# Kernel tuning notes

Measured on AMD Instinct MI355X. Metric: run time of the kernel, lower is better.

The kernel has to match this reference:

```python
import jax, jax.numpy as jnp
import numpy as np


def setup_inputs() -> dict:
    key = jax.random.key(0)
    ks = jax.random.split(key, 12)
    N_DRUGS, D, N_CELLS, C_IN, E = 4096, 128, 1024, 1000, 500000
    inp = {
        "drug_hidden_out": jax.random.normal(ks[0], (N_DRUGS, D), dtype=jnp.float32),
        "cell_hidden_out": jax.random.normal(ks[1], (N_CELLS, C_IN), dtype=jnp.float32),
        # columns: drug1_idx, drug2_idx, cell_idx, label (original code indexes
        # drug_hidden_out with ALL THREE index columns, so bound by N_DRUGS)
        "all_edges": jax.random.randint(ks[2], (E, 4), 0, N_DRUGS, dtype=jnp.int64),
        # proj: Linear(1000, 128)
        "proj_W": jax.random.normal(ks[3], (D, C_IN), dtype=jnp.float32) * 0.03,
        "proj_b": jnp.zeros((D,), dtype=jnp.float32),
        # NN: Linear(128,32) -> ReLU -> Linear(32,32) -> ReLU -> Linear(32,32)
        #     -> ReLU -> Dropout(eval=identity) -> Linear(32,1) -> Sigmoid
        "W1": jax.random.normal(ks[4], (32, D), dtype=jnp.float32) * 0.08,
        "b1": jnp.zeros((32,), dtype=jnp.float32),
        "W2": jax.random.normal(ks[5], (32, 32), dtype=jnp.float32) * 0.17,
        "b2": jnp.zeros((32,), dtype=jnp.float32),
        "W3": jax.random.normal(ks[6], (32, 32), dtype=jnp.float32) * 0.17,
        "b3": jnp.zeros((32,), dtype=jnp.float32),
        "W4": jax.random.normal(ks[7], (1, 32), dtype=jnp.float32) * 0.17,
        "b4": jnp.zeros((1,), dtype=jnp.float32),
    }
    return inp


def reference(drug_hidden_out, cell_hidden_out, all_edges,
              proj_W, proj_b, W1, b1, W2, b2, W3, b3, W4, b4):
    # proj is computed in the original forward but its result is never used
    # downstream (the code re-indexes drug_hidden_out for cell_fea).
    _cell_proj = cell_hidden_out @ proj_W.T + proj_b  # [n_cells, 128], dead value

    edges = all_edges.T                 # [4, E]
    label = edges[3]                    # [E]
    edge_index = edges[:3]              # [3, E]

    drug1_fea = drug_hidden_out[edge_index[0]]   # [E, 128] gather
    drug2_fea = drug_hidden_out[edge_index[1]]   # [E, 128] gather
    cell_fea = drug_hidden_out[edge_index[2]]    # [E, 128] gather (faithful to source bug)
    logits = drug1_fea * drug2_fea * cell_fea    # [E, 128]

    h = jax.nn.relu(logits @ W1.T + b1)          # [E, 32]
    h = jax.nn.relu(h @ W2.T + b2)               # [E, 32]
    h = jax.nn.relu(h @ W3.T + b3)               # [E, 32] (dropout = identity in eval)
    x = jax.nn.sigmoid(h @ W4.T + b4)            # [E, 1]
    return x, label
```

## Files before the change

### kernel.cpp

```cpp
#include <hip/hip_runtime.h>
#include <stdint.h>

#define DD 128
#define HH 32
#define TABQ (4096 * DD / 4)
#define BLOB_OFF (1u << 20)

typedef _Float16 f16;
typedef _Float16 f16x2 __attribute__((ext_vector_type(2)));
typedef _Float16 f16x4 __attribute__((ext_vector_type(4)));
typedef _Float16 f16x8 __attribute__((ext_vector_type(8)));
typedef float    f32x4 __attribute__((ext_vector_type(4)));
typedef uint32_t u32x4 __attribute__((ext_vector_type(4)));

#define GL1(p)  ((const __attribute__((address_space(1))) void*)(p))
#define LDS3(p) ((__attribute__((address_space(3))) void*)(p))

__global__ __launch_bounds__(256)
void synergy_prepass(const float* __restrict__ drug,
                     const float* __restrict__ W1, const float* __restrict__ W2,
                     const float* __restrict__ W3, const float* __restrict__ W4,
                     f16* __restrict__ tab)
{
    const int tid = threadIdx.x;
    if ((int)blockIdx.x == 512) {
        f16x8* __restrict__ blob16 = (f16x8*)((char*)tab + BLOB_OFF);
        const float4* __restrict__ W1v = (const float4*)W1;
        #pragma unroll
        for (int p = 0; p < 2; ++p) {
            const int S = p * 256 + tid;
            const int t = S >> 8, f = (S >> 6) & 3, l = S & 63;
            const int mm = l & 15, qq = l >> 4;
            const int c4 = (t * 16 + mm) * (DD / 4) + f * 8 + qq * 2;
            const float4 w0 = W1v[c4], w1 = W1v[c4 + 1];
            f16x8 r;
            r[0]=(f16)w0.x; r[1]=(f16)w0.y; r[2]=(f16)w0.z; r[3]=(f16)w0.w;
            r[4]=(f16)w1.x; r[5]=(f16)w1.y; r[6]=(f16)w1.z; r[7]=(f16)w1.w;
            blob16[S] = r;
        }
        {
            const int B = tid & 127;
            const int t = B >> 6, l = B & 63;
            const int mm = l & 15, qq = l >> 4;
            const int c4 = (t * 16 + mm) * (HH / 4) + qq * 2;
            const float4* __restrict__ src = (tid < 128) ? (const float4*)W2 : (const float4*)W3;
            const float4 w0 = src[c4], w1 = src[c4 + 1];
            f16x8 r;
            r[0]=(f16)w0.x; r[1]=(f16)w0.y; r[2]=(f16)w0.z; r[3]=(f16)w0.w;
            r[4]=(f16)w1.x; r[5]=(f16)w1.y; r[6]=(f16)w1.z; r[7]=(f16)w1.w;
            blob16[512 + (tid & 128) + B] = r;
        }
        if (tid < 64) {
            const int mm = tid & 15, qq = tid >> 4;
            f16x8 r;
            #pragma unroll
            for (int j = 0; j < 8; ++j)
                r[j] = (mm == 0) ? (f16)W4[qq * 8 + j] : (f16)0.0f;
            blob16[768 + tid] = r;
        }
        return;
    }
    const int i = blockIdx.x * 256 + tid;
    if (i < TABQ) {
        const float4 v = ((const float4*)drug)[i];
        f16x4 h;
        h[0]=(f16)v.x; h[1]=(f16)v.y; h[2]=(f16)v.z; h[3]=(f16)v.w;
        ((f16x4*)tab)[i] = h;
    }
}

static __device__ __forceinline__ uint32_t pkh(float a, float b) {
    f16x2 h; h[0] = (f16)a; h[1] = (f16)b;
    return __builtin_bit_cast(uint32_t, h);
}
static __device__ __forceinline__ void plswap32(uint32_t &a, uint32_t &b) {
#if __has_builtin(__builtin_amdgcn_permlane32_swap)
    auto r = __builtin_amdgcn_permlane32_swap(a, b, false, false);
    a = r[0]; b = r[1];
#else
    asm volatile("v_permlane32_swap_b32 %0, %1" : "+v"(a), "+v"(b));
#endif
}
static __device__ __forceinline__ void plswap16(uint32_t &a, uint32_t &b) {
#if __has_builtin(__builtin_amdgcn_permlane16_swap)
    auto r = __builtin_amdgcn_permlane16_swap(a, b, false, false);
    a = r[0]; b = r[1];
#else
    asm volatile("v_permlane16_swap_b32 %0, %1" : "+v"(a), "+v"(b));
#endif
}

static __device__ __forceinline__ void pin4(f16x8 &w) {
    u32x4 t = __builtin_bit_cast(u32x4, w);
    asm volatile("" : "+v"(t));
    w = __builtin_bit_cast(f16x8, t);
}

static __device__ __forceinline__ f16x8 transition(f32x4 a0, f32x4 a1) {
    uint32_t u0 = pkh(fmaxf(a0[0], 0.f), fmaxf(a0[1], 0.f));
    uint32_t u1 = pkh(fmaxf(a0[2], 0.f), fmaxf(a0[3], 0.f));
    uint32_t v0 = pkh(fmaxf(a1[0], 0.f), fmaxf(a1[1], 0.f));
    uint32_t v1 = pkh(fmaxf(a1[2], 0.f), fmaxf(a1[3], 0.f));
    plswap32(u0, v0);
    plswap32(u1, v1);
    plswap16(u0, v0);
    plswap16(u1, v1);
    u32x4 d; d[0] = u0; d[1] = u1; d[2] = v0; d[3] = v1;
    return __builtin_bit_cast(f16x8, d);
}

__global__ __launch_bounds__(256, 3)
void synergy_main(const f16* __restrict__ tab, const int* __restrict__ edges,
                  const float* __restrict__ b1, const float* __restrict__ b2,
                  const float* __restrict__ b3, const float* __restrict__ b4,
                  float* __restrict__ out, int E, int NG)
{
    __shared__ __align__(16) f16 stage[4][6144];
    __shared__ __align__(16) float blds[96];

    const int tid  = threadIdx.x;
    const int wave = tid >> 6;
    const int lane = tid & 63;
    const int m    = lane & 15;
    const int q    = lane >> 4;

    const char* __restrict__ tabB   = (const char*)tab;
    const f16x8* __restrict__ blobG = (const f16x8*)(tabB + BLOB_OFF);

    if (tid < 96) {
        const float* __restrict__ src = (tid < 32) ? b1 : ((tid < 64) ? b2 : b3);
        blds[tid] = src[tid & 31];
    }
    __syncthreads();

    const int WSTR = (int)gridDim.x * 4;
    int g = (int)blockIdx.x * 4 + wave;
    if (g >= NG) return;

    f16x8 w1a[4], w1b[4];
    #pragma unroll
    for (int f = 0; f < 4; ++f) {
        w1a[f] = blobG[f * 64 + lane];
        w1b[f] = blobG[256 + f * 64 + lane];
    }
    f16x8 w2a = blobG[512 + lane], w2b = blobG[576 + lane];
    f16x8 w3a = blobG[640 + lane], w3b = blobG[704 + lane];
    f16x8 wf4 = blobG[768 + lane];
    #pragma unroll
    for (int f = 0; f < 4; ++f) { pin4(w1a[f]); pin4(w1b[f]); }
    pin4(w2a); pin4(w2b); pin4(w3a); pin4(w3b); pin4(wf4);
    const float b4v = b4[0];

    f16* __restrict__ stg = stage[wave];
    const int4* __restrict__ edges4 = (const int4*)edges;

    auto load_ed = [&](int gg) -> int4 {
        int e = (gg << 4) + m;
        e = (e < E) ? e : (E - 1);
        return edges4[e];
    };
    auto issue_dma = [&](const int4 ed) {
        int rowb[12];
        #pragma unroll
        for (int gg = 0; gg < 4; ++gg) {
            const int src = 4 * gg + q;
            rowb[0 * 4 + gg] = __shfl(ed.x, src, 64) << 8;
            rowb[1 * 4 + gg] = __shfl(ed.y, src, 64) << 8;
            rowb[2 * 4 + gg] = __shfl(ed.z, src, 64) << 8;
        }
        __builtin_amdgcn_sched_barrier(0);
        #pragma unroll
        for (int t = 0; t < 3; ++t)
            #pragma unroll
            for (int gg = 0; gg < 4; ++gg) {
                const int seg16 = ((m + 4 * gg + q) & 15) << 4;
                __builtin_amdgcn_global_load_lds(
                    GL1(tabB + (size_t)(rowb[t * 4 + gg] + seg16)),
                    LDS3((char*)stg + (t * 16 + 4 * gg) * 256), 16, 0, 0);
            }
    };

    int4 ed_cur = load_ed(g);
    issue_dma(ed_cur);
    int gn = g + WSTR;
    int4 ed_nxt = load_ed((gn < NG) ? gn : g);

    int wzero = 0;
    for (;;) {
        __builtin_amdgcn_s_waitcnt(0x0F70);
        __builtin_amdgcn_sched_barrier(0);
        asm volatile("" : "+v"(wzero));
        const f32x4* __restrict__ bl = (const f32x4*)blds + wzero;

        f32x4 acc0 = bl[q];
        f32x4 acc1 = bl[4 + q];
        #pragma unroll
        for (int f = 0; f < 4; ++f) {
            const int slot = (((f * 4 + q) - m) & 15) << 3;
            const f16x8 v0 = *(const f16x8*)(stg + (0 * 16 + m) * 128 + slot);
            const f16x8 v1 = *(const f16x8*)(stg + (1 * 16 + m) * 128 + slot);
            const f16x8 v2 = *(const f16x8*)(stg + (2 * 16 + m) * 128 + slot);
            const f16x8 p = v0 * v1 * v2;
            acc0 = __builtin_amdgcn_mfma_f32_16x16x32_f16(w1a[f], p, acc0, 0, 0, 0);
            acc1 = __builtin_amdgcn_mfma_f32_16x16x32_f16(w1b[f], p, acc1, 0, 0, 0);
        }
        const f16x8 h1 = transition(acc0, acc1);

        const int gf = gn + WSTR;
        const int4 ed_fut = load_ed((gf < NG) ? gf : g);

        f32x4 c0 = bl[8 + q];
        f32x4 c1 = bl[12 + q];
        c0 = __builtin_amdgcn_mfma_f32_16x16x32_f16(w2a, h1, c0, 0, 0, 0);
        c1 = __builtin_amdgcn_mfma_f32_16x16x32_f16(w2b, h1, c1, 0, 0, 0);
        const f16x8 h2 = transition(c0, c1);

        f32x4 d0 = bl[16 + q];
        f32x4 d1 = bl[20 + q];
        d0 = __builtin_amdgcn_mfma_f32_16x16x32_f16(w3a, h2, d0, 0, 0, 0);
        d1 = __builtin_amdgcn_mfma_f32_16x16x32_f16(w3b, h2, d1, 0, 0, 0);
        const f16x8 h3 = transition(d0, d1);

        {
            f32x4 z = {b4v, b4v, b4v, b4v};
            z = __builtin_amdgcn_mfma_f32_16x16x32_f16(wf4, h3, z, 0, 0, 0);
            if (q == 0) {
                const int e0 = (g << 4) + m;
                if (e0 < E) out[e0] = 1.0f / (1.0f + __expf(-z[0]));
            }
        }
        const int eL = (g << 4) + lane;
        if (lane < 16 && eL < E) out[E + eL] = (float)ed_cur.w;

        if (gn >= NG) break;
        issue_dma(ed_nxt);
        g = gn; gn = gf; ed_cur = ed_nxt; ed_nxt = ed_fut;
    }
}

extern "C" void kernel_launch(void* const* d_in, const int* in_sizes, int n_in,
                              void* d_out, int out_size, void* d_ws, size_t ws_size,
                              hipStream_t stream)
{
    const float* drug  = (const float*)d_in[0];
    const int*   edges = (const int*)d_in[2];
    const float* W1 = (const float*)d_in[5];
    const float* b1 = (const float*)d_in[6];
    const float* W2 = (const float*)d_in[7];
    const float* b2 = (const float*)d_in[8];
    const float* W3 = (const float*)d_in[9];
    const float* b3 = (const float*)d_in[10];
    const float* W4 = (const float*)d_in[11];
    const float* b4 = (const float*)d_in[12];
    float* out = (float*)d_out;
    f16*   tab = (f16*)d_ws;

    const int E  = in_sizes[2] / 4;
    const int NG = (E + 15) / 16;

    hipLaunchKernelGGL(synergy_prepass, dim3(513), dim3(256), 0, stream,
                       drug, W1, W2, W3, W4, tab);
    int blocks = (NG + 3) / 4;
    if (blocks > 768) blocks = 768;
    hipLaunchKernelGGL(synergy_main, dim3(blocks), dim3(256), 0, stream,
                       tab, edges, b1, b2, b3, b4, out, E, NG);
}
```

Before: 114.6 us.

## Issue next gather DMA right after layer-1 reads and keep biases in registers

```diff
diff --git a/kernel.cpp b/kernel.cpp
--- a/kernel.cpp
+++ b/kernel.cpp
@@ -95,6 +95,9 @@
     asm volatile("" : "+v"(t));
     w = __builtin_bit_cast(f16x8, t);
 }
+static __device__ __forceinline__ void pin4f(f32x4 &w) {
+    asm volatile("" : "+v"(w));
+}
 
 static __device__ __forceinline__ f16x8 transition(f32x4 a0, f32x4 a1) {
     uint32_t u0 = pkh(fmaxf(a0[0], 0.f), fmaxf(a0[1], 0.f));
@@ -116,7 +119,6 @@
                   float* __restrict__ out, int E, int NG)
 {
     __shared__ __align__(16) f16 stage[4][6144];
-    __shared__ __align__(16) float blds[96];
 
     const int tid  = threadIdx.x;
     const int wave = tid >> 6;
@@ -126,12 +128,6 @@
 
     const char* __restrict__ tabB   = (const char*)tab;
     const f16x8* __restrict__ blobG = (const f16x8*)(tabB + BLOB_OFF);
-
-    if (tid < 96) {
-        const float* __restrict__ src = (tid < 32) ? b1 : ((tid < 64) ? b2 : b3);
-        blds[tid] = src[tid & 31];
-    }
-    __syncthreads();
 
     const int WSTR = (int)gridDim.x * 4;
     int g = (int)blockIdx.x * 4 + wave;
@@ -149,6 +145,11 @@
     #pragma unroll
     for (int f = 0; f < 4; ++f) { pin4(w1a[f]); pin4(w1b[f]); }
     pin4(w2a); pin4(w2b); pin4(w3a); pin4(w3b); pin4(wf4);
+
+    f32x4 bb1a = *(const f32x4*)(b1 + 4 * q), bb1b = *(const f32x4*)(b1 + 16 + 4 * q);
+    f32x4 bb2a = *(const f32x4*)(b2 + 4 * q), bb2b = *(const f32x4*)(b2 + 16 + 4 * q);
+    f32x4 bb3a = *(const f32x4*)(b3 + 4 * q), bb3b = *(const f32x4*)(b3 + 16 + 4 * q);
+    pin4f(bb1a); pin4f(bb1b); pin4f(bb2a); pin4f(bb2b); pin4f(bb3a); pin4f(bb3b);
     const float b4v = b4[0];
 
     f16* __restrict__ stg = stage[wave];
@@ -178,22 +179,22 @@
                     GL1(tabB + (size_t)(rowb[t * 4 + gg] + seg16)),
                     LDS3((char*)stg + (t * 16 + 4 * gg) * 256), 16, 0, 0);
             }
+        __builtin_amdgcn_sched_barrier(0);
     };
 
     int4 ed_cur = load_ed(g);
     issue_dma(ed_cur);
     int gn = g + WSTR;
     int4 ed_nxt = load_ed((gn < NG) ? gn : g);
-
-    int wzero = 0;
+    __builtin_amdgcn_s_waitcnt(0x0F70);
+    __builtin_amdgcn_sched_barrier(0);
+
     for (;;) {
-        __builtin_amdgcn_s_waitcnt(0x0F70);
+        __builtin_amdgcn_s_waitcnt(0x0F73);
         __builtin_amdgcn_sched_barrier(0);
-        asm volatile("" : "+v"(wzero));
-        const f32x4* __restrict__ bl = (const f32x4*)blds + wzero;
-
-        f32x4 acc0 = bl[q];
-        f32x4 acc1 = bl[4 + q];
+
+        f32x4 acc0 = bb1a;
+        f32x4 acc1 = bb1b;
         #pragma unroll
         for (int f = 0; f < 4; ++f) {
             const int slot = (((f * 4 + q) - m) & 15) << 3;
@@ -206,17 +207,22 @@
         }
         const f16x8 h1 = transition(acc0, acc1);
 
+        const bool last = (gn >= NG);
         const int gf = gn + WSTR;
-        const int4 ed_fut = load_ed((gf < NG) ? gf : g);
-
-        f32x4 c0 = bl[8 + q];
-        f32x4 c1 = bl[12 + q];
+        int4 ed_fut = ed_nxt;
+        if (!last) {
+            issue_dma(ed_nxt);
+            ed_fut = load_ed((gf < NG) ? gf : g);
+        }
+
+        f32x4 c0 = bb2a;
+        f32x4 c1 = bb2b;
         c0 = __builtin_amdgcn_mfma_f32_16x16x32_f16(w2a, h1, c0, 0, 0, 0);
         c1 = __builtin_amdgcn_mfma_f32_16x16x32_f16(w2b, h1, c1, 0, 0, 0);
         const f16x8 h2 = transition(c0, c1);
 
-        f32x4 d0 = bl[16 + q];
-        f32x4 d1 = bl[20 + q];
+        f32x4 d0 = bb3a;
+        f32x4 d1 = bb3b;
         d0 = __builtin_amdgcn_mfma_f32_16x16x32_f16(w3a, h2, d0, 0, 0, 0);
         d1 = __builtin_amdgcn_mfma_f32_16x16x32_f16(w3b, h2, d1, 0, 0, 0);
         const f16x8 h3 = transition(d0, d1);
@@ -232,8 +238,7 @@
         const int eL = (g << 4) + lane;
         if (lane < 16 && eL < E) out[E + eL] = (float)ed_cur.w;
 
-        if (gn >= NG) break;
-        issue_dma(ed_nxt);
+        if (last) break;
         g = gn; gn = gf; ed_cur = ed_nxt; ed_nxt = ed_fut;
     }
 }
```

Result: faster. 111.8 us (-2.4%).
